# Kernel optimization log

Hardware: AMD Instinct MI355X
Metric: run time of the kernel (lower is better)

The kernel has to match this reference:

```python
import jax, jax.numpy as jnp
import numpy as np

B, N, C = 64, 197, 768
H = 12
N_TOK = 118
CUTOFF = 0.15


def setup_inputs() -> dict:
    key = jax.random.key(0)
    ks = jax.random.split(key, 6)
    s = 0.02
    return {
        "x": jax.random.normal(ks[0], (B, N, C), jnp.float32),
        "ln1_w": jnp.ones((C,), jnp.float32),
        "ln1_b": jnp.zeros((C,), jnp.float32),
        "qkv_w": jax.random.normal(ks[1], (3 * C, C), jnp.float32) * s,
        "proj_w": jax.random.normal(ks[2], (C, C), jnp.float32) * s,
        "proj_b": jnp.zeros((C,), jnp.float32),
        "gamma1": jnp.ones((C,), jnp.float32),
        "ln2_w": jnp.ones((C,), jnp.float32),
        "ln2_b": jnp.zeros((C,), jnp.float32),
        "fc1_w": jax.random.normal(ks[3], (4 * C, C), jnp.float32) * s,
        "fc1_b": jnp.zeros((4 * C,), jnp.float32),
        "fc2_w": jax.random.normal(ks[4], (C, 4 * C), jnp.float32) * s,
        "fc2_b": jnp.zeros((C,), jnp.float32),
        "gamma2": jnp.ones((C,), jnp.float32),
    }


def _ln(x, w, b, eps=1e-5):
    m = x.mean(-1, keepdims=True)
    v = ((x - m) ** 2).mean(-1, keepdims=True)
    return (x - m) / jnp.sqrt(v + eps) * w + b


def _attention(x, qkv_w, proj_w, proj_b):
    Bx, Nx, Cx = x.shape
    dh = Cx // H
    qkv = x @ qkv_w.T                                    # [B,N,3C]
    qk = qkv[:, :, : 2 * Cx].reshape(Bx, Nx, 2, H, dh).transpose(2, 0, 3, 1, 4)
    q, k = qk[0], qk[1]                                  # [B,H,N,dh]
    v = qkv[:, :, 2 * Cx :].reshape(Bx, Nx, H, dh).transpose(0, 2, 1, 3)
    attn = jax.nn.softmax((q * dh ** -0.5) @ k.transpose(0, 1, 3, 2), axis=-1)  # [B,H,N,N]
    out = (attn @ v).transpose(0, 2, 1, 3).reshape(Bx, Nx, Cx)
    return out @ proj_w.T + proj_b, attn


def _selector(x, attn, n_tokens, cutoff):
    # attention-weighted scores
    cls_aw = attn[:, :, 1:, 0].mean(-1)[..., None]        # [B,H,1]
    cls_attn = (attn[:, :, 0, 1:] * cls_aw).mean(1)       # [B,N-1]
    img_aw = attn[:, :, 0, 0][..., None]                  # [B,H,1]
    img_attn = (attn[:, :, 1:, 1:].mean(2) * img_aw).mean(1)
    token_attn = cls_attn + img_attn                      # [B,N-1]
    # FFT low-frequency-energy score (detached in original)
    img_token = jax.lax.stop_gradient(x[:, 1:].astype(jnp.float32).transpose(0, 2, 1))  # [B,C,N-1]
    f = jnp.fft.fft(img_token, axis=-1)
    amp = jnp.abs(f)
    pha = jnp.angle(f)
    L = img_token.shape[-1]
    d0 = (L * cutoff / 2.0) ** 2
    m0 = (L - 1) / 2.0
    grid = jnp.arange(L, dtype=jnp.float32)
    kernel = 1.0 - jnp.exp(-((grid - m0) ** 2) / (2.0 * d0))  # high-pass notch
    amp = amp * kernel
    f2 = amp * jnp.cos(pha) + 1j * amp * jnp.sin(pha)
    tok = jnp.fft.ifft(f2, axis=-1)                       # [B,C,N-1] complex
    token_lfe = jnp.abs(tok).sum(1) / jnp.abs(img_token).sum(1).mean(-1)[..., None]
    scores = token_lfe * token_attn                        # [B,N-1]
    _, idx = jax.lax.top_k(scores, n_tokens)               # [B,n_tokens]
    Cx = x.shape[-1]
    sav = jnp.take_along_axis(x[:, 1:], idx[:, :, None], axis=1)  # [B,n_tokens,C]
    return jnp.concatenate([x[:, 0:1], sav], axis=1)


def reference(x, ln1_w, ln1_b, qkv_w, proj_w, proj_b, gamma1,
              ln2_w, ln2_b, fc1_w, fc1_b, fc2_w, fc2_b, gamma2):
    x_msa, attn = _attention(_ln(x, ln1_w, ln1_b), qkv_w, proj_w, proj_b)
    x = gamma1 * x_msa + x
    x = _selector(x, attn, N_TOK, CUTOFF)                 # [B,1+N_TOK,C]
    h = _ln(x, ln2_w, ln2_b)
    h = jax.nn.gelu(h @ fc1_w.T + fc1_b, approximate=False)
    h = h @ fc2_w.T + fc2_b
    return gamma2 * h + x
```

## Files before the change

kernel.cpp:

```cpp
#include <hip/hip_runtime.h>
#include <math.h>

#define NTOK 197
#define NIMG 196
#define CDIM 768
#define NHEAD 12
#define HD 64
#define BATCH 64
#define NSEL 118
#define ROWS_FULL (BATCH*NTOK)
#define ROWS_SEL  (BATCH*(NSEL+1))

typedef short bf16x8 __attribute__((ext_vector_type(8)));
typedef float f32x4  __attribute__((ext_vector_type(4)));

#define GLDS(g, l) __builtin_amdgcn_global_load_lds( \
    (const __attribute__((address_space(1))) void*)(g), \
    (__attribute__((address_space(3))) void*)(l), 16, 0, 0)

__device__ __forceinline__ unsigned short f2bf(float f){
  union { float f; unsigned u; } v; v.f = f;
  unsigned r = v.u + 0x7FFF + ((v.u >> 16) & 1);
  return (unsigned short)(r >> 16);
}
__device__ __forceinline__ float bf2f(unsigned short h){
  union { unsigned u; float f; } v; v.u = ((unsigned)h) << 16; return v.f;
}

template<int OUT>
__global__ __launch_bounds__(256) void ln_kernel(
    const float* __restrict__ x, const float* __restrict__ w,
    const float* __restrict__ b, void* __restrict__ outv)
{
  const int row = blockIdx.x;
  const int t = threadIdx.x;
  const float* xr = x + (size_t)row * CDIM;
  float v0 = xr[t], v1 = xr[t+256], v2 = xr[t+512];
  float s = v0 + v1 + v2;
  __shared__ float red[4], red2[4];
  #pragma unroll
  for (int o=32;o>0;o>>=1) s += __shfl_down(s,o);
  if ((t&63)==0) red[t>>6] = s;
  __syncthreads();
  const float mean = (red[0]+red[1]+red[2]+red[3]) / 768.0f;
  const float d0=v0-mean, d1=v1-mean, d2=v2-mean;
  float vs = d0*d0 + d1*d1 + d2*d2;
  #pragma unroll
  for (int o=32;o>0;o>>=1) vs += __shfl_down(vs,o);
  if ((t&63)==0) red2[t>>6] = vs;
  __syncthreads();
  const float var = (red2[0]+red2[1]+red2[2]+red2[3]) / 768.0f;
  const float rstd = 1.0f / sqrtf(var + 1e-5f);
  const float o0 = d0*rstd*w[t]     + b[t];
  const float o1 = d1*rstd*w[t+256] + b[t+256];
  const float o2 = d2*rstd*w[t+512] + b[t+512];
  if (OUT == 0){
    float* orow = (float*)outv + (size_t)row * CDIM;
    orow[t] = o0; orow[t+256] = o1; orow[t+512] = o2;
  } else {
    unsigned short* orow = (unsigned short*)outv + (size_t)row * CDIM;
    orow[t] = f2bf(o0); orow[t+256] = f2bf(o1); orow[t+512] = f2bf(o2);
  }
}

__global__ __launch_bounds__(256) void ln_split3_kernel(
    const float* __restrict__ x, const float* __restrict__ w,
    const float* __restrict__ b, unsigned short* __restrict__ dst, size_t plane)
{
  const int row = blockIdx.x;
  const int t = threadIdx.x;
  const float* xr = x + (size_t)row * CDIM;
  float v0 = xr[t], v1 = xr[t+256], v2 = xr[t+512];
  float s = v0 + v1 + v2;
  __shared__ float red[4], red2[4];
  #pragma unroll
  for (int o=32;o>0;o>>=1) s += __shfl_down(s,o);
  if ((t&63)==0) red[t>>6] = s;
  __syncthreads();
  const float mean = (red[0]+red[1]+red[2]+red[3]) / 768.0f;
  const float d0=v0-mean, d1=v1-mean, d2=v2-mean;
  float vs = d0*d0 + d1*d1 + d2*d2;
  #pragma unroll
  for (int o=32;o>0;o>>=1) vs += __shfl_down(vs,o);
  if ((t&63)==0) red2[t>>6] = vs;
  __syncthreads();
  const float var = (red2[0]+red2[1]+red2[2]+red2[3]) / 768.0f;
  const float rstd = 1.0f / sqrtf(var + 1e-5f);
  const float ov[3] = { d0*rstd*w[t]     + b[t],
                        d1*rstd*w[t+256] + b[t+256],
                        d2*rstd*w[t+512] + b[t+512] };
  #pragma unroll
  for (int e=0;e<3;e++){
    const int col = t + e*256;
    const float f = ov[e];
    const unsigned short p0 = f2bf(f);
    const float r1 = f - bf2f(p0);
    const unsigned short p1 = f2bf(r1);
    const unsigned short p2 = f2bf(r1 - bf2f(p1));
    dst[(size_t)row*CDIM + col]             = p0;
    dst[plane + (size_t)row*CDIM + col]     = p1;
    dst[2*plane + (size_t)row*CDIM + col]   = p2;
  }
}

__global__ __launch_bounds__(256) void cvt_bf16_kernel(
    const float* __restrict__ src, unsigned short* __restrict__ dst, int n4)
{
  const int i = blockIdx.x*256 + threadIdx.x;
  if (i < n4){
    const float4 v = *(const float4*)(src + (size_t)i*4);
    dst[(size_t)i*4+0] = f2bf(v.x); dst[(size_t)i*4+1] = f2bf(v.y);
    dst[(size_t)i*4+2] = f2bf(v.z); dst[(size_t)i*4+3] = f2bf(v.w);
  }
}

__global__ __launch_bounds__(192) void cvt3_kernel(
    const float* __restrict__ w, unsigned short* __restrict__ W3, int K)
{
  const int n = blockIdx.x, t = threadIdx.x;
  const float4 v = *(const float4*)(w + (size_t)n*K + t*4);
  ushort4 hi, lo;
  hi.x = f2bf(v.x); lo.x = f2bf(v.x - bf2f(hi.x));
  hi.y = f2bf(v.y); lo.y = f2bf(v.y - bf2f(hi.y));
  hi.z = f2bf(v.z); lo.z = f2bf(v.z - bf2f(hi.z));
  hi.w = f2bf(v.w); lo.w = f2bf(v.w - bf2f(hi.w));
  *(ushort4*)(W3 + (size_t)n*2*K + t*4)     = hi;
  *(ushort4*)(W3 + (size_t)n*2*K + K + t*4) = lo;
}

__global__ __launch_bounds__(256) void cvt_split3_kernel(
    const float* __restrict__ src, unsigned short* __restrict__ dst,
    int n4, size_t plane)
{
  const int i = blockIdx.x*256 + threadIdx.x;
  if (i >= n4) return;
  const float4 v = *(const float4*)(src + (size_t)i*4);
  const float f[4] = {v.x, v.y, v.z, v.w};
  unsigned short p0[4], p1[4], p2[4];
  #pragma unroll
  for (int q=0;q<4;q++){
    p0[q] = f2bf(f[q]);
    const float r1 = f[q] - bf2f(p0[q]);
    p1[q] = f2bf(r1);
    const float r2 = r1 - bf2f(p1[q]);
    p2[q] = f2bf(r2);
  }
  *(ushort4*)(dst + (size_t)i*4)           = make_ushort4(p0[0],p0[1],p0[2],p0[3]);
  *(ushort4*)(dst + plane + (size_t)i*4)   = make_ushort4(p1[0],p1[1],p1[2],p1[3]);
  *(ushort4*)(dst + 2*plane + (size_t)i*4) = make_ushort4(p2[0],p2[1],p2[2],p2[3]);
}

__global__ __launch_bounds__(256) void gemm_f32_kernel(
    const float* __restrict__ A, const float* __restrict__ W,
    float* __restrict__ out, int M, int N, int K)
{
  __shared__ float As[16][132];
  __shared__ float Bs[16][132];
  const int t  = threadIdx.x;
  const int tx = t & 15, ty = t >> 4;
  const int m0 = blockIdx.x * 128, n0 = blockIdx.y * 128;
  const int lr = t >> 2, lc = (t & 3) << 2;
  float acc[2][2][4][4] = {{{{0.f}}}};
  const float4 z4 = make_float4(0.f,0.f,0.f,0.f);
  const int rowA0 = m0 + lr, rowA1 = m0 + 64 + lr;
  const size_t strA0 = (size_t)rowA0 * K, strA1 = (size_t)rowA1 * K;
  const size_t strW0 = (size_t)(n0+lr) * K, strW1 = (size_t)(n0+64+lr) * K;
  for (int k0=0; k0<K; k0+=16){
    float4 a0 = (rowA0 < M) ? *(const float4*)(A + strA0 + k0 + lc) : z4;
    float4 a1 = (rowA1 < M) ? *(const float4*)(A + strA1 + k0 + lc) : z4;
    float4 w0 = *(const float4*)(W + strW0 + k0 + lc);
    float4 w1 = *(const float4*)(W + strW1 + k0 + lc);
    __syncthreads();
    As[lc+0][lr]=a0.x; As[lc+1][lr]=a0.y; As[lc+2][lr]=a0.z; As[lc+3][lr]=a0.w;
    As[lc+0][64+lr]=a1.x; As[lc+1][64+lr]=a1.y; As[lc+2][64+lr]=a1.z; As[lc+3][64+lr]=a1.w;
    Bs[lc+0][lr]=w0.x; Bs[lc+1][lr]=w0.y; Bs[lc+2][lr]=w0.z; Bs[lc+3][lr]=w0.w;
    Bs[lc+0][64+lr]=w1.x; Bs[lc+1][64+lr]=w1.y; Bs[lc+2][64+lr]=w1.z; Bs[lc+3][64+lr]=w1.w;
    __syncthreads();
    #pragma unroll
    for (int k=0;k<16;k++){
      const float4 av0 = *(const float4*)&As[k][ty*4];
      const float4 av1 = *(const float4*)&As[k][64+ty*4];
      const float4 bv0 = *(const float4*)&Bs[k][tx*4];
      const float4 bv1 = *(const float4*)&Bs[k][64+tx*4];
      const float ar[2][4] = {{av0.x,av0.y,av0.z,av0.w},{av1.x,av1.y,av1.z,av1.w}};
      const float br[2][4] = {{bv0.x,bv0.y,bv0.z,bv0.w},{bv1.x,bv1.y,bv1.z,bv1.w}};
      #pragma unroll
      for (int ri=0;ri<2;ri++)
        #pragma unroll
        for (int i=0;i<4;i++)
          #pragma unroll
          for (int ci=0;ci<2;ci++)
            #pragma unroll
            for (int j=0;j<4;j++)
              acc[ri][ci][i][j] = fmaf(ar[ri][i], br[ci][j], acc[ri][ci][i][j]);
    }
  }
  #pragma unroll
  for (int ri=0;ri<2;ri++){
    #pragma unroll
    for (int i=0;i<4;i++){
      const int row = m0 + ri*64 + ty*4 + i;
      if (row >= M) continue;
      #pragma unroll
      for (int ci=0;ci<2;ci++){
        const int col = n0 + ci*64 + tx*4;
        *(float4*)(out + (size_t)row*N + col) =
          make_float4(acc[ri][ci][i][0],acc[ri][ci][i][1],acc[ri][ci][i][2],acc[ri][ci][i][3]);
      }
    }
  }
}

__global__ __launch_bounds__(512) void mfma_gemm6w_kernel(
    const unsigned short* __restrict__ A3, const unsigned short* __restrict__ W3,
    float* __restrict__ out, int M, int N, int K, size_t planeA, size_t planeW,
    int gx)
{
  __shared__ __align__(16) unsigned short As[3][64*64];
  __shared__ __align__(16) unsigned short Ws[256*64];
  const int nwg = gridDim.x;
  const int q8 = nwg >> 3, r8 = nwg & 7;
  const int xcd = blockIdx.x & 7, lid = blockIdx.x >> 3;
  const int swz = (xcd < r8) ? (xcd*(q8+1) + lid) : (r8*(q8+1) + (xcd-r8)*q8 + lid);
  const int bx = swz % gx, by = swz / gx;

  const int t = threadIdx.x;
  const int w = t >> 6, lane = t & 63;
  const int m0 = bx * 64, n0 = by * 256;
  const int wr = w >> 2, wc = w & 3;
  f32x4 acc[2][4];
  #pragma unroll
  for (int i=0;i<2;i++)
    #pragma unroll
    for (int j=0;j<4;j++){ acc[i][j][0]=0.f; acc[i][j][1]=0.f; acc[i][j][2]=0.f; acc[i][j][3]=0.f; }

  const int srow = lane >> 3;
  const int slot = lane & 7;
  const int scol = (slot ^ srow) * 8;
  const int aloc = w*8;
  const int wloc = w*32;
  const int fr = lane & 15;
  const int kg = lane >> 4;

  #define SEGW(NA)                                                            \
    _Pragma("unroll")                                                         \
    for (int ksub = 0; ksub < 2; ksub++){                                     \
      const int kbyte = ksub*64 + kg*16;                                      \
      bf16x8 b[4];                                                            \
      _Pragma("unroll")                                                       \
      for (int ni=0; ni<4; ni++){                                             \
        const int br = wc*64 + ni*16 + fr;                                    \
        b[ni] = *(const bf16x8*)(Ws + br*64 + ((kbyte ^ ((br&7)<<4)) >> 1));  \
      }                                                                       \
      _Pragma("unroll")                                                       \
      for (int p=0; p<NA; p++){                                               \
        bf16x8 a[2];                                                          \
        _Pragma("unroll")                                                     \
        for (int mi=0; mi<2; mi++){                                           \
          const int ar = wr*32 + mi*16 + fr;                                  \
          a[mi] = *(const bf16x8*)(As[p] + ar*64 + ((kbyte ^ ((ar&7)<<4)) >> 1)); \
        }                                                                     \
        _Pragma("unroll")                                                     \
        for (int mi=0; mi<2; mi++)                                            \
          _Pragma("unroll")                                                   \
          for (int ni=0; ni<4; ni++)                                          \
            acc[mi][ni] = __builtin_amdgcn_mfma_f32_16x16x32_bf16(a[mi], b[ni], acc[mi][ni], 0, 0, 0); \
      }                                                                       \
    }

  #define STAGE_W(P)                                                          \
    _Pragma("unroll")                                                         \
    for (int tt=0; tt<4; tt++){                                               \
      const int rl = wloc + tt*8;                                             \
      GLDS(W3 + (size_t)(P)*planeW + (size_t)(n0+rl+srow)*K + k0 + scol, Ws + rl*64); \
    }

  for (int k0 = 0; k0 < K; k0 += 64){
    __syncthreads();
    #pragma unroll
    for (int p=0; p<3; p++)
      GLDS(A3 + (size_t)p*planeA + (size_t)(m0+aloc+srow)*K + k0 + scol, As[p] + aloc*64);
    STAGE_W(0)
    __syncthreads();
    SEGW(3)
    __syncthreads();
    STAGE_W(1)
    __syncthreads();
    SEGW(2)
    __syncthreads();
    STAGE_W(2)
    __syncthreads();
    SEGW(1)
  }
  #undef SEGW
  #undef STAGE_W

  const int cL = lane & 15, rL = lane >> 4;
  #pragma unroll
  for (int mi=0; mi<2; mi++){
    #pragma unroll
    for (int ni=0; ni<4; ni++){
      const int col = n0 + wc*64 + ni*16 + cL;
      const int rowb = m0 + wr*32 + mi*16 + rL*4;
      #pragma unroll
      for (int r=0; r<4; r++){
        const int row = rowb + r;
        if (row >= M) continue;
        out[(size_t)row*N + col] = acc[mi][ni][r];
      }
    }
  }
}

template<int EPI>
__global__ __launch_bounds__(512) void mfma_gemm1w_kernel(
    const unsigned short* __restrict__ A, const unsigned short* __restrict__ W,
    const float* __restrict__ bias, const float* __restrict__ gamma,
    const float* __restrict__ resid, void* __restrict__ outv,
    int M, int N, int K, int gx)
{
  __shared__ __align__(16) unsigned short As[64*64];
  __shared__ __align__(16) unsigned short Ws[256*64];
  const int nwg = gridDim.x;
  const int q8 = nwg >> 3, r8 = nwg & 7;
  const int xcd = blockIdx.x & 7, lid = blockIdx.x >> 3;
  const int swz = (xcd < r8) ? (xcd*(q8+1) + lid) : (r8*(q8+1) + (xcd-r8)*q8 + lid);
  const int bx = swz % gx, by = swz / gx;

  const int t = threadIdx.x;
  const int w = t >> 6, lane = t & 63;
  const int m0 = bx * 64, n0 = by * 256;
  const int wr = w >> 2, wc = w & 3;
  f32x4 acc[2][4];
  #pragma unroll
  for (int i=0;i<2;i++)
    #pragma unroll
    for (int j=0;j<4;j++){ acc[i][j][0]=0.f; acc[i][j][1]=0.f; acc[i][j][2]=0.f; acc[i][j][3]=0.f; }

  const int srow = lane >> 3;
  const int slot = lane & 7;
  const int scol = (slot ^ srow) * 8;
  const int aloc = w*8;
  const int wloc = w*32;
  const int fr = lane & 15;
  const int kg = lane >> 4;

  for (int k0 = 0; k0 < K; k0 += 64){
    __syncthreads();
    GLDS(A + (size_t)(m0+aloc+srow)*K + k0 + scol, As + aloc*64);
    #pragma unroll
    for (int tt=0; tt<4; tt++){
      const int rl = wloc + tt*8;
      GLDS(W + (size_t)(n0+rl+srow)*K + k0 + scol, Ws + rl*64);
    }
    __syncthreads();
    #pragma unroll
    for (int ksub = 0; ksub < 2; ksub++){
      const int kbyte = ksub*64 + kg*16;
      bf16x8 b[4];
      #pragma unroll
      for (int ni=0; ni<4; ni++){
        const int br = wc*64 + ni*16 + fr;
        b[ni] = *(const bf16x8*)(Ws + br*64 + ((kbyte ^ ((br&7)<<4)) >> 1));
      }
      bf16x8 a[2];
      #pragma unroll
      for (int mi=0; mi<2; mi++){
        const int ar = wr*32 + mi*16 + fr;
        a[mi] = *(const bf16x8*)(As + ar*64 + ((kbyte ^ ((ar&7)<<4)) >> 1));
      }
      #pragma unroll
      for (int mi=0; mi<2; mi++)
        #pragma unroll
        for (int ni=0; ni<4; ni++)
          acc[mi][ni] = __builtin_amdgcn_mfma_f32_16x16x32_bf16(a[mi], b[ni], acc[mi][ni], 0, 0, 0);
    }
  }

  const int cL = lane & 15, rL = lane >> 4;
  #pragma unroll
  for (int mi=0; mi<2; mi++){
    #pragma unroll
    for (int ni=0; ni<4; ni++){
      const int col = n0 + wc*64 + ni*16 + cL;
      const int rowb = m0 + wr*32 + mi*16 + rL*4;
      const float bb = bias[col];
      #pragma unroll
      for (int r=0; r<4; r++){
        const int row = rowb + r;
        if (row >= M) continue;
        float v = acc[mi][ni][r] + bb;
        if (EPI == 2){
          v = 0.5f*v*(1.0f + erff(v*0.7071067811865475f));
          ((unsigned short*)outv)[(size_t)row*N + col] = f2bf(v);
        } else {
          v = gamma[col]*v + resid[(size_t)row*N + col];
          ((float*)outv)[(size_t)row*N + col] = v;
        }
      }
    }
  }
}

__global__ __launch_bounds__(512) void mfma_proj3_kernel(
    const unsigned short* __restrict__ A, const unsigned short* __restrict__ W,
    const float* __restrict__ bias, const float* __restrict__ gamma,
    const float* __restrict__ resid, float* __restrict__ out,
    int M, int N, int K, int gx)
{
  __shared__ __align__(16) unsigned short Ah[64*64], Al[64*64];
  __shared__ __align__(16) unsigned short Ws[256*64];
  const int nwg = gridDim.x;
  const int q8 = nwg >> 3, r8 = nwg & 7;
  const int xcd = blockIdx.x & 7, lid = blockIdx.x >> 3;
  const int swz = (xcd < r8) ? (xcd*(q8+1) + lid) : (r8*(q8+1) + (xcd-r8)*q8 + lid);
  const int bx = swz % gx, by = swz / gx;

  const int t = threadIdx.x;
  const int w = t >> 6, lane = t & 63;
  const int m0 = bx * 64, n0 = by * 256;
  const int wr = w >> 2, wc = w & 3;
  const int lda = 2*K;
  f32x4 acc[2][4];
  #pragma unroll
  for (int i=0;i<2;i++)
    #pragma unroll
    for (int j=0;j<4;j++){ acc[i][j][0]=0.f; acc[i][j][1]=0.f; acc[i][j][2]=0.f; acc[i][j][3]=0.f; }

  const int srow = lane >> 3;
  const int slot = lane & 7;
  const int scol = (slot ^ srow) * 8;
  const int aloc = w*8;
  const int wloc = w*32;
  const int fr = lane & 15;
  const int kg = lane >> 4;

  #define PSEG(NA)                                                            \
    _Pragma("unroll")                                                         \
    for (int ksub = 0; ksub < 2; ksub++){                                     \
      const int kbyte = ksub*64 + kg*16;                                      \
      bf16x8 b[4];                                                            \
      _Pragma("unroll")                                                       \
      for (int ni=0; ni<4; ni++){                                             \
        const int br = wc*64 + ni*16 + fr;                                    \
        b[ni] = *(const bf16x8*)(Ws + br*64 + ((kbyte ^ ((br&7)<<4)) >> 1));  \
      }                                                                       \
      _Pragma("unroll")                                                       \
      for (int mi=0; mi<2; mi++){                                             \
        const int ar = wr*32 + mi*16 + fr;                                    \
        const int ao = ar*64 + ((kbyte ^ ((ar&7)<<4)) >> 1);                  \
        bf16x8 ah = *(const bf16x8*)(Ah + ao);                                \
        _Pragma("unroll")                                                     \
        for (int ni=0; ni<4; ni++)                                            \
          acc[mi][ni] = __builtin_amdgcn_mfma_f32_16x16x32_bf16(ah, b[ni], acc[mi][ni], 0, 0, 0); \
        if (NA > 1){                                                          \
          bf16x8 al = *(const bf16x8*)(Al + ao);                              \
          _Pragma("unroll")                                                   \
          for (int ni=0; ni<4; ni++)                                          \
            acc[mi][ni] = __builtin_amdgcn_mfma_f32_16x16x32_bf16(al, b[ni], acc[mi][ni], 0, 0, 0); \
        }                                                                     \
      }                                                                       \
    }

  for (int k0 = 0; k0 < K; k0 += 64){
    __syncthreads();
    {
      const size_t abase = (size_t)(m0+aloc+srow)*lda + k0 + scol;
      GLDS(A + abase,     Ah + aloc*64);
      GLDS(A + abase + K, Al + aloc*64);
    }
    #pragma unroll
    for (int tt=0; tt<4; tt++){
      const int rl = wloc + tt*8;
      GLDS(W + (size_t)(n0+rl+srow)*lda + k0 + scol, Ws + rl*64);
    }
    __syncthreads();
    PSEG(2)
    __syncthreads();
    #pragma unroll
    for (int tt=0; tt<4; tt++){
      const int rl = wloc + tt*8;
      GLDS(W + (size_t)(n0+rl+srow)*lda + K + k0 + scol, Ws + rl*64);
    }
    __syncthreads();
    PSEG(1)
  }
  #undef PSEG

  const int cL = lane & 15, rL = lane >> 4;
  #pragma unroll
  for (int mi=0; mi<2; mi++){
    #pragma unroll
    for (int ni=0; ni<4; ni++){
      const int col = n0 + wc*64 + ni*16 + cL;
      const int rowb = m0 + wr*32 + mi*16 + rL*4;
      const float bb = bias[col];
      const float gg = gamma[col];
      #pragma unroll
      for (int r=0; r<4; r++){
        const int row = rowb + r;
        if (row >= M) continue;
        out[(size_t)row*N + col] = gg*(acc[mi][ni][r] + bb) + resid[(size_t)row*N + col];
      }
    }
  }
}

__global__ __launch_bounds__(256) void attn_fused_kernel(
    const float* __restrict__ qkv, double* __restrict__ mbuf,
    double* __restrict__ lbuf, unsigned short* __restrict__ msa3)
{
  __shared__ float Kt[NTOK][HD];
  __shared__ float Vt[NTOK][HD];
  __shared__ double q0s[HD];
  __shared__ float m0sh;
  __shared__ double red[4];
  __shared__ float l0f;
  const int bh = blockIdx.x;
  const int b = bh / NHEAD, h = bh % NHEAD;
  const float* basep = qkv + (size_t)b*NTOK*2304 + h*HD;
  for (int li=threadIdx.x; li<NTOK*16; li+=256){
    const int r = li >> 4, c4 = (li & 15) << 2;
    *(float4*)&Kt[r][c4] = *(const float4*)(basep + (size_t)r*2304 +  768 + c4);
    *(float4*)&Vt[r][c4] = *(const float4*)(basep + (size_t)r*2304 + 1536 + c4);
  }
  if (threadIdx.x < 16){
    const float4 t4 = *(const float4*)(basep + threadIdx.x*4);
    q0s[threadIdx.x*4+0] = (double)t4.x*0.125; q0s[threadIdx.x*4+1] = (double)t4.y*0.125;
    q0s[threadIdx.x*4+2] = (double)t4.z*0.125; q0s[threadIdx.x*4+3] = (double)t4.w*0.125;
  }
  __syncthreads();
  const int i = threadIdx.x;
  float4 q[16];
  float m = -INFINITY, linv = 0.f;
  if (i < NTOK){
    #pragma unroll
    for (int dd=0; dd<16; dd++){
      float4 tq = *(const float4*)(basep + (size_t)i*2304 + dd*4);
      q[dd] = make_float4(tq.x*0.125f, tq.y*0.125f, tq.z*0.125f, tq.w*0.125f);
    }
    float l = 0.f;
    for (int j=0;j<NTOK;j++){
      float s = 0.f;
      #pragma unroll
      for (int dd=0;dd<16;dd++){
        const float4 kk = *(const float4*)&Kt[j][dd*4];
        s = fmaf(q[dd].x,kk.x,s); s = fmaf(q[dd].y,kk.y,s);
        s = fmaf(q[dd].z,kk.z,s); s = fmaf(q[dd].w,kk.w,s);
      }
      const float mn = fmaxf(m, s);
      l = l*expf(m-mn) + expf(s-mn);
      m = mn;
    }
    mbuf[bh*NTOK+i] = (double)m;
    linv = 1.0f/l;
    if (i > 0) lbuf[bh*NTOK+i] = (double)linv;
    if (i == 0) m0sh = m;
  }
  __syncthreads();
  double e = 0.0;
  if (i < NTOK){
    double s64 = 0.0;
    #pragma unroll
    for (int d=0; d<HD; d++) s64 = fma(q0s[d], (double)Kt[i][d], s64);
    e = exp(s64 - (double)m0sh);
  }
  #pragma unroll
  for (int o=32;o>0;o>>=1) e += __shfl_down(e,o);
  if ((i&63)==0) red[i>>6] = e;
  __syncthreads();
  if (i==0){
    const double l0 = 1.0/(red[0]+red[1]+red[2]+red[3]);
    lbuf[bh*NTOK] = l0;
    l0f = (float)l0;
  }
  __syncthreads();
  if (i >= NTOK) return;
  if (i == 0) linv = l0f;
  float4 o[16];
  #pragma unroll
  for (int dd=0;dd<16;dd++) o[dd] = make_float4(0.f,0.f,0.f,0.f);
  for (int j=0;j<NTOK;j++){
    float s = 0.f;
    #pragma unroll
    for (int dd=0;dd<16;dd++){
      const float4 kk = *(const float4*)&Kt[j][dd*4];
      s = fmaf(q[dd].x,kk.x,s); s = fmaf(q[dd].y,kk.y,s);
      s = fmaf(q[dd].z,kk.z,s); s = fmaf(q[dd].w,kk.w,s);
    }
    const float p = expf(s - m) * linv;
    #pragma unroll
    for (int dd=0;dd<16;dd++){
      const float4 vv = *(const float4*)&Vt[j][dd*4];
      o[dd].x = fmaf(p,vv.x,o[dd].x); o[dd].y = fmaf(p,vv.y,o[dd].y);
      o[dd].z = fmaf(p,vv.z,o[dd].z); o[dd].w = fmaf(p,vv.w,o[dd].w);
    }
  }
  unsigned short* orow = msa3 + ((size_t)b*NTOK + i)*1536 + h*HD;
  #pragma unroll
  for (int dd=0;dd<16;dd++){
    const float4 v = o[dd];
    ushort4 hi, lo;
    hi.x = f2bf(v.x); lo.x = f2bf(v.x - bf2f(hi.x));
    hi.y = f2bf(v.y); lo.y = f2bf(v.y - bf2f(hi.y));
    hi.z = f2bf(v.z); lo.z = f2bf(v.z - bf2f(hi.z));
    hi.w = f2bf(v.w); lo.w = f2bf(v.w - bf2f(hi.w));
    *(ushort4*)(orow + dd*4)       = hi;
    *(ushort4*)(orow + 768 + dd*4) = lo;
  }
}

__global__ __launch_bounds__(256) void attn_sel_kernel(
    const float* __restrict__ qkv, const double* __restrict__ mbuf,
    const double* __restrict__ lbuf, double* __restrict__ ta_part)
{
  __shared__ float Qt[NTOK][HD];
  __shared__ double q0s[HD];
  __shared__ float msf[NTOK], lsf[NTOK];
  __shared__ double m0d, l0inv;
  __shared__ double sh_cs0, sh_r00;
  const int bh = blockIdx.x;
  const int b = bh / NHEAD, h = bh % NHEAD;
  const float* basep = qkv + (size_t)b*NTOK*2304 + h*HD;
  for (int li=threadIdx.x; li<NTOK*16; li+=256){
    const int r = li >> 4, c4 = (li & 15) << 2;
    float4 tq = *(const float4*)(basep + (size_t)r*2304 + c4);
    Qt[r][c4+0]=tq.x*0.125f; Qt[r][c4+1]=tq.y*0.125f;
    Qt[r][c4+2]=tq.z*0.125f; Qt[r][c4+3]=tq.w*0.125f;
  }
  if (threadIdx.x < 16){
    const float4 t4 = *(const float4*)(basep + threadIdx.x*4);
    q0s[threadIdx.x*4+0] = (double)t4.x*0.125; q0s[threadIdx.x*4+1] = (double)t4.y*0.125;
    q0s[threadIdx.x*4+2] = (double)t4.z*0.125; q0s[threadIdx.x*4+3] = (double)t4.w*0.125;
  }
  for (int li=threadIdx.x; li<NTOK; li+=256){
    msf[li] = (float)mbuf[bh*NTOK+li];
    lsf[li] = (float)lbuf[bh*NTOK+li];
  }
  if (threadIdx.x == 0){ m0d = mbuf[bh*NTOK]; l0inv = lbuf[bh*NTOK]; }
  __syncthreads();
  const int j = threadIdx.x;
  double colsum = 0.0, row0 = 0.0;
  if (j < NTOK){
    float4 kreg[16];
    #pragma unroll
    for (int dd=0;dd<16;dd++) kreg[dd] = *(const float4*)(basep + (size_t)j*2304 + 768 + dd*4);
    {
      double s64 = 0.0;
      #pragma unroll
      for (int dd=0;dd<16;dd++){
        s64 = fma(q0s[dd*4+0], (double)kreg[dd].x, s64);
        s64 = fma(q0s[dd*4+1], (double)kreg[dd].y, s64);
        s64 = fma(q0s[dd*4+2], (double)kreg[dd].z, s64);
        s64 = fma(q0s[dd*4+3], (double)kreg[dd].w, s64);
      }
      row0 = exp(s64 - m0d) * l0inv;
    }
    for (int i2=1;i2<NTOK;i2++){
      float s = 0.f;
      #pragma unroll
      for (int dd=0;dd<16;dd++){
        const float4 qq = *(const float4*)&Qt[i2][dd*4];
        s = fmaf(qq.x,kreg[dd].x,s); s = fmaf(qq.y,kreg[dd].y,s);
        s = fmaf(qq.z,kreg[dd].z,s); s = fmaf(qq.w,kreg[dd].w,s);
      }
      colsum += (double)(expf(s - msf[i2]) * lsf[i2]);
    }
  }
  if (j == 0){ sh_cs0 = colsum; sh_r00 = row0; }
  __syncthreads();
  if (j >= 1 && j < NTOK){
    ta_part[(size_t)bh*NIMG + (j-1)] = row0 * (sh_cs0 / 196.0) + (colsum / 196.0) * sh_r00;
  }
}

__global__ __launch_bounds__(256) void reduce_ta_kernel(
    const double* __restrict__ ta_part, double* __restrict__ token_attn)
{
  const int b = blockIdx.x, j = threadIdx.x;
  if (j < NIMG){
    double s = 0.0;
    for (int h=0; h<NHEAD; h++) s += ta_part[((size_t)b*NHEAD + h)*NIMG + j];
    token_attn[b*NIMG + j] = s / 12.0;
  }
}

__global__ __launch_bounds__(256) void circ_kernel(float* __restrict__ circ)
{
  const int d = blockIdx.x;
  const int g = threadIdx.x;
  __shared__ double rs[4], is[4];
  double re = 0.0, im = 0.0;
  if (g < NIMG){
    const double d0   = (196.0 * 0.15 / 2.0);
    const double twod = 2.0 * d0 * d0;
    const double gg = (double)g - 97.5;
    const double kg = 1.0 - exp(-(gg*gg)/twod);
    const int gd = (g*d) % NIMG;
    const double ang = 6.283185307179586476925286766559 * ((double)gd / 196.0);
    re = kg * cos(ang);
    im = kg * sin(ang);
  }
  #pragma unroll
  for (int o=32;o>0;o>>=1){ re += __shfl_down(re,o); im += __shfl_down(im,o); }
  if ((g&63)==0){ rs[g>>6] = re; is[g>>6] = im; }
  __syncthreads();
  if (g == 0){
    circ[d]        = (float)((rs[0]+rs[1]+rs[2]+rs[3]) / 196.0);
    circ[NIMG + d] = (float)((is[0]+is[1]+is[2]+is[3]) / 196.0);
  }
}

__global__ __launch_bounds__(256) void lfe_kernel(
    const float* __restrict__ x1, const float* __restrict__ circ,
    double* __restrict__ lfe_part, double* __restrict__ den_part)
{
  __shared__ float xs[NIMG][36];
  __shared__ float2 c2[NIMG];
  __shared__ double red[4];
  const int cg = blockIdx.x, b = blockIdx.y;
  const int c0 = cg * 32;
  for (int li=threadIdx.x; li<NIMG*32; li+=256){
    const int m = li >> 5, ch = li & 31;
    xs[m][ch] = x1[((size_t)b*NTOK + 1 + m)*CDIM + c0 + ch];
  }
  for (int li=threadIdx.x; li<NIMG; li+=256) c2[li] = make_float2(circ[li], circ[NIMG+li]);
  __syncthreads();
  const int n = threadIdx.x;
  double lfe_sum = 0.0, den_sum = 0.0;
  if (n < NIMG){
    #pragma unroll 1
    for (int g=0; g<4; g++){
      const int cc0 = g*8;
      float re[8] = {0,0,0,0,0,0,0,0};
      float im[8] = {0,0,0,0,0,0,0,0};
      int d = n;
      for (int mm=0; mm<NIMG; mm++){
        const float2 cc = c2[d];
        const float4 xa = *(const float4*)&xs[mm][cc0];
        const float4 xb = *(const float4*)&xs[mm][cc0+4];
        const float xv[8] = {xa.x,xa.y,xa.z,xa.w,xb.x,xb.y,xb.z,xb.w};
        #pragma unroll
        for (int q=0;q<8;q++){
          re[q] = fmaf(cc.x, xv[q], re[q]);
          im[q] = fmaf(cc.y, xv[q], im[q]);
        }
        d = (d==0) ? (NIMG-1) : (d-1);
      }
      #pragma unroll
      for (int q=0;q<8;q++) lfe_sum += (double)sqrtf(re[q]*re[q] + im[q]*im[q]);
    }
    #pragma unroll
    for (int q=0;q<8;q++){
      const float4 xv = *(const float4*)&xs[n][q*4];
      den_sum += (double)fabsf(xv.x)+(double)fabsf(xv.y)+(double)fabsf(xv.z)+(double)fabsf(xv.w);
    }
    lfe_part[((size_t)b*24 + cg)*NIMG + n] = lfe_sum;
  }
  double s = (n < NIMG) ? den_sum : 0.0;
  #pragma unroll
  for (int o=32;o>0;o>>=1) s += __shfl_down(s,o);
  if ((threadIdx.x & 63) == 0) red[threadIdx.x >> 6] = s;
  __syncthreads();
  if (threadIdx.x == 0) den_part[b*24 + cg] = red[0]+red[1]+red[2]+red[3];
}

__global__ __launch_bounds__(256) void scores_kernel(
    const double* __restrict__ lfe_part, const double* __restrict__ den_part,
    const double* __restrict__ token_attn, double* __restrict__ scores)
{
  const int b = blockIdx.x, n = threadIdx.x;
  if (n < NIMG){
    double num = 0.0;
    for (int cg=0; cg<24; cg++) num += lfe_part[((size_t)b*24 + cg)*NIMG + n];
    double den = 0.0;
    for (int cg=0; cg<24; cg++) den += den_part[b*24 + cg];
    const double tl = num / (den / 196.0);
    scores[b*NIMG + n] = tl * token_attn[b*NIMG + n];
  }
}

__global__ void topk_kernel(const double* __restrict__ scores, int* __restrict__ idx)
{
  __shared__ double w[NIMG];
  const int b = blockIdx.x, lane = threadIdx.x;
  for (int i=lane; i<NIMG; i+=64) w[i] = scores[b*NIMG + i];
  __syncthreads();
  for (int r=0; r<NSEL; r++){
    double bv = -INFINITY; int bi = NIMG;
    for (int i=lane; i<NIMG; i+=64){
      const double v = w[i];
      if (v > bv){ bv = v; bi = i; }
    }
    #pragma unroll
    for (int o=32;o>0;o>>=1){
      const double ov = __shfl_down(bv,o);
      const int    oi = __shfl_down(bi,o);
      if (ov > bv || (ov == bv && oi < bi)){ bv = ov; bi = oi; }
    }
    if (lane == 0){
      idx[b*NSEL + r] = bi;
      w[bi] = -INFINITY;
    }
    __syncthreads();
  }
}

__global__ void gather_kernel(const float* __restrict__ x1, const int* __restrict__ idx,
                              float* __restrict__ xsel)
{
  const int row = blockIdx.x;
  const int b = row / (NSEL+1), r = row % (NSEL+1);
  const int src = (r == 0) ? 0 : (1 + idx[b*NSEL + (r-1)]);
  const float4* s = (const float4*)(x1 + ((size_t)b*NTOK + src)*CDIM);
  float4* d = (float4*)(xsel + (size_t)row*CDIM);
  d[threadIdx.x] = s[threadIdx.x];
}

extern "C" void kernel_launch(void* const* d_in, const int* in_sizes, int n_in,
                              void* d_out, int out_size, void* d_ws, size_t ws_size,
                              hipStream_t stream)
{
  const float* x      = (const float*)d_in[0];
  const float* ln1_w  = (const float*)d_in[1];
  const float* ln1_b  = (const float*)d_in[2];
  const float* qkv_w  = (const float*)d_in[3];
  const float* proj_w = (const float*)d_in[4];
  const float* proj_b = (const float*)d_in[5];
  const float* gamma1 = (const float*)d_in[6];
  const float* ln2_w  = (const float*)d_in[7];
  const float* ln2_b  = (const float*)d_in[8];
  const float* fc1_w  = (const float*)d_in[9];
  const float* fc1_b  = (const float*)d_in[10];
  const float* fc2_w  = (const float*)d_in[11];
  const float* fc2_b  = (const float*)d_in[12];
  const float* gamma2 = (const float*)d_in[13];
  float* out = (float*)d_out;
  float* ws  = (float*)d_ws;

  float* R1 = ws;
  float* R2 = ws + 9732096;
  double* D = (double*)(ws + 9732096 + 29048832);
  double* mbuf = D;
  double* lbuf = mbuf + 151296;
  double* tap  = lbuf + 151296;
  double* ta   = tap  + 150528;
  double* lfep = ta   + 12544;
  double* denp = lfep + 301056;
  double* sc   = denp + 1536;
  float* circ  = (float*)(sc + 12544);
  int*   idxb  = (int*)(circ + 392);
  unsigned short* W3p = (unsigned short*)(ws + 40350472);
  unsigned short* WQ3 = (unsigned short*)(ws + 40940296);
  unsigned short* XQ3 = (unsigned short*)(ws + 43594504);
  const size_t NEED_BYTES = (size_t)58192648 * 4;

  float* xln  = R1;
  unsigned short* msa3 = (unsigned short*)R1;
  float* xsel = R1;
  float* qkv  = R2;
  float* x1   = R2;
  unsigned short* ln2o_bf = (unsigned short*)(R2 + 9682944);
  unsigned short* fc1w_bf = (unsigned short*)(R2 + 12632064);
  unsigned short* fc2w_bf = (unsigned short*)(R2 + 13811712);
  unsigned short* h1_bf   = (unsigned short*)(R2 + 14991360);

  if (ws_size >= NEED_BYTES){
    ln_split3_kernel<<<ROWS_FULL, 256, 0, stream>>>(x, ln1_w, ln1_b, XQ3, (size_t)9732096);
    cvt_split3_kernel<<<(442368+255)/256, 256, 0, stream>>>(qkv_w, WQ3, 442368, (size_t)1769472);
    mfma_gemm6w_kernel<<<197*9, 512, 0, stream>>>(XQ3, WQ3, qkv, ROWS_FULL, 2304, 768,
                                                  (size_t)9732096, (size_t)1769472, 197);
  } else {
    ln_kernel<0><<<ROWS_FULL, 256, 0, stream>>>(x, ln1_w, ln1_b, xln);
    gemm_f32_kernel<<<dim3(99,18), 256, 0, stream>>>(xln, qkv_w, qkv, ROWS_FULL, 2304, 768);
  }
  attn_fused_kernel<<<BATCH*NHEAD, 256, 0, stream>>>(qkv, mbuf, lbuf, msa3);
  attn_sel_kernel<<<BATCH*NHEAD, 256, 0, stream>>>(qkv, mbuf, lbuf, tap);
  reduce_ta_kernel<<<BATCH, 256, 0, stream>>>(tap, ta);
  cvt3_kernel<<<CDIM, 192, 0, stream>>>(proj_w, W3p, CDIM);
  mfma_proj3_kernel<<<197*3, 512, 0, stream>>>(msa3, W3p, proj_b, gamma1, x,
                                               x1, ROWS_FULL, CDIM, CDIM, 197);
  cvt_bf16_kernel<<<2304, 256, 0, stream>>>(fc1_w, fc1w_bf, 589824);
  cvt_bf16_kernel<<<2304, 256, 0, stream>>>(fc2_w, fc2w_bf, 589824);
  circ_kernel<<<NIMG, 256, 0, stream>>>(circ);
  lfe_kernel<<<dim3(24, BATCH), 256, 0, stream>>>(x1, circ, lfep, denp);
  scores_kernel<<<BATCH, 256, 0, stream>>>(lfep, denp, ta, sc);
  topk_kernel<<<BATCH, 64, 0, stream>>>(sc, idxb);
  gather_kernel<<<ROWS_SEL, 192, 0, stream>>>(x1, idxb, xsel);
  ln_kernel<1><<<ROWS_SEL, 256, 0, stream>>>(xsel, ln2_w, ln2_b, ln2o_bf);
  mfma_gemm1w_kernel<2><<<119*12, 512, 0, stream>>>(ln2o_bf, fc1w_bf, fc1_b, nullptr,
                                                    nullptr, h1_bf, ROWS_SEL, 3072, 768, 119);
  mfma_gemm1w_kernel<3><<<119*3, 512, 0, stream>>>(h1_bf, fc2w_bf, fc2_b, gamma2,
                                                   xsel, out, ROWS_SEL, 768, 3072, 119);
}
```

Baseline: 1.395 ms.

## Fuse attention into single-pass online softmax with direct V reads

Replaces the two-pass attention (first computing row max/sum, then recomputing QK scores to accumulate P·V) with a single-pass online-softmax loop that rescales the output accumulator whenever the running max changes. V is no longer staged in shared memory and is read directly from global memory (broadcast across threads), halving LDS use and possibly raising occupancy. This removes the duplicated QK dot products, but adds conditional rescaling work, per-thread uniform global loads of V, and higher register pressure from keeping q and o live together.

```diff
diff --git a/kernel.cpp b/kernel.cpp
--- a/kernel.cpp
+++ b/kernel.cpp
@@ -506,12 +506,11 @@
   }
 }
 
-__global__ __launch_bounds__(256) void attn_fused_kernel(
+__global__ __launch_bounds__(256) void attn_flash_kernel(
     const float* __restrict__ qkv, double* __restrict__ mbuf,
     double* __restrict__ lbuf, unsigned short* __restrict__ msa3)
 {
   __shared__ float Kt[NTOK][HD];
-  __shared__ float Vt[NTOK][HD];
   __shared__ double q0s[HD];
   __shared__ float m0sh;
   __shared__ double red[4];
@@ -521,8 +520,7 @@
   const float* basep = qkv + (size_t)b*NTOK*2304 + h*HD;
   for (int li=threadIdx.x; li<NTOK*16; li+=256){
     const int r = li >> 4, c4 = (li & 15) << 2;
-    *(float4*)&Kt[r][c4] = *(const float4*)(basep + (size_t)r*2304 +  768 + c4);
-    *(float4*)&Vt[r][c4] = *(const float4*)(basep + (size_t)r*2304 + 1536 + c4);
+    *(float4*)&Kt[r][c4] = *(const float4*)(basep + (size_t)r*2304 + 768 + c4);
   }
   if (threadIdx.x < 16){
     const float4 t4 = *(const float4*)(basep + threadIdx.x*4);
@@ -532,14 +530,15 @@
   __syncthreads();
   const int i = threadIdx.x;
   float4 q[16];
-  float m = -INFINITY, linv = 0.f;
+  float4 o[16];
+  float m = -INFINITY, l = 0.f;
   if (i < NTOK){
     #pragma unroll
     for (int dd=0; dd<16; dd++){
       float4 tq = *(const float4*)(basep + (size_t)i*2304 + dd*4);
       q[dd] = make_float4(tq.x*0.125f, tq.y*0.125f, tq.z*0.125f, tq.w*0.125f);
-    }
-    float l = 0.f;
+      o[dd] = make_float4(0.f,0.f,0.f,0.f);
+    }
     for (int j=0;j<NTOK;j++){
       float s = 0.f;
       #pragma unroll
@@ -549,12 +548,26 @@
         s = fmaf(q[dd].z,kk.z,s); s = fmaf(q[dd].w,kk.w,s);
       }
       const float mn = fmaxf(m, s);
-      l = l*expf(m-mn) + expf(s-mn);
+      const float sc = expf(m - mn);
+      const float p  = expf(s - mn);
+      l = l*sc + p;
+      if (sc != 1.0f){
+        #pragma unroll
+        for (int dd=0;dd<16;dd++){
+          o[dd].x *= sc; o[dd].y *= sc; o[dd].z *= sc; o[dd].w *= sc;
+        }
+      }
       m = mn;
+      const float* vrow = basep + (size_t)j*2304 + 1536;
+      #pragma unroll
+      for (int dd=0;dd<16;dd++){
+        const float4 vv = *(const float4*)(vrow + dd*4);
+        o[dd].x = fmaf(p,vv.x,o[dd].x); o[dd].y = fmaf(p,vv.y,o[dd].y);
+        o[dd].z = fmaf(p,vv.z,o[dd].z); o[dd].w = fmaf(p,vv.w,o[dd].w);
+      }
     }
     mbuf[bh*NTOK+i] = (double)m;
-    linv = 1.0f/l;
-    if (i > 0) lbuf[bh*NTOK+i] = (double)linv;
+    if (i > 0) lbuf[bh*NTOK+i] = (double)(1.0f/l);
     if (i == 0) m0sh = m;
   }
   __syncthreads();
@@ -566,7 +579,7 @@
     e = exp(s64 - (double)m0sh);
   }
   #pragma unroll
-  for (int o=32;o>0;o>>=1) e += __shfl_down(e,o);
+  for (int o2=32;o2>0;o2>>=1) e += __shfl_down(e,o2);
   if ((i&63)==0) red[i>>6] = e;
   __syncthreads();
   if (i==0){
@@ -576,30 +589,11 @@
   }
   __syncthreads();
   if (i >= NTOK) return;
-  if (i == 0) linv = l0f;
-  float4 o[16];
-  #pragma unroll
-  for (int dd=0;dd<16;dd++) o[dd] = make_float4(0.f,0.f,0.f,0.f);
-  for (int j=0;j<NTOK;j++){
-    float s = 0.f;
-    #pragma unroll
-    for (int dd=0;dd<16;dd++){
-      const float4 kk = *(const float4*)&Kt[j][dd*4];
-      s = fmaf(q[dd].x,kk.x,s); s = fmaf(q[dd].y,kk.y,s);
-      s = fmaf(q[dd].z,kk.z,s); s = fmaf(q[dd].w,kk.w,s);
-    }
-    const float p = expf(s - m) * linv;
-    #pragma unroll
-    for (int dd=0;dd<16;dd++){
-      const float4 vv = *(const float4*)&Vt[j][dd*4];
-      o[dd].x = fmaf(p,vv.x,o[dd].x); o[dd].y = fmaf(p,vv.y,o[dd].y);
-      o[dd].z = fmaf(p,vv.z,o[dd].z); o[dd].w = fmaf(p,vv.w,o[dd].w);
-    }
-  }
+  const float linv = (i == 0) ? l0f : (1.0f/l);
   unsigned short* orow = msa3 + ((size_t)b*NTOK + i)*1536 + h*HD;
   #pragma unroll
   for (int dd=0;dd<16;dd++){
-    const float4 v = o[dd];
+    const float4 v = make_float4(o[dd].x*linv, o[dd].y*linv, o[dd].z*linv, o[dd].w*linv);
     ushort4 hi, lo;
     hi.x = f2bf(v.x); lo.x = f2bf(v.x - bf2f(hi.x));
     hi.y = f2bf(v.y); lo.y = f2bf(v.y - bf2f(hi.y));
@@ -874,7 +868,7 @@
     ln_kernel<0><<<ROWS_FULL, 256, 0, stream>>>(x, ln1_w, ln1_b, xln);
     gemm_f32_kernel<<<dim3(99,18), 256, 0, stream>>>(xln, qkv_w, qkv, ROWS_FULL, 2304, 768);
   }
-  attn_fused_kernel<<<BATCH*NHEAD, 256, 0, stream>>>(qkv, mbuf, lbuf, msa3);
+  attn_flash_kernel<<<BATCH*NHEAD, 256, 0, stream>>>(qkv, mbuf, lbuf, msa3);
   attn_sel_kernel<<<BATCH*NHEAD, 256, 0, stream>>>(qkv, mbuf, lbuf, tap);
   reduce_ta_kernel<<<BATCH, 256, 0, stream>>>(tap, ta);
   cvt3_kernel<<<CDIM, 192, 0, stream>>>(proj_w, W3p, CDIM);
```

Measured after the change: 1.266 ms, median of 2. -9.2%, faster.
